# Kernel optimization log

Measured on AMD Instinct MI355X. Metric: run time of the kernel, lower is better.

The kernel has to match this reference:

```python
import jax, jax.numpy as jnp
import numpy as np

NUM_EMBEDDINGS = 1024
EMBEDDING_DIM = 512
COMMITMENT_COST = 0.25


def setup_inputs() -> dict:
    key = jax.random.key(0)
    k1, k2 = jax.random.split(key)
    inputs = jax.random.normal(k1, (128, 512, EMBEDDING_DIM), dtype=jnp.float32)
    # torch init: uniform_(-1/K, 1/K)
    emb_weight = jax.random.uniform(
        k2, (NUM_EMBEDDINGS, EMBEDDING_DIM), dtype=jnp.float32,
        minval=-1.0 / NUM_EMBEDDINGS, maxval=1.0 / NUM_EMBEDDINGS)
    return {"inputs": inputs, "emb_weight": emb_weight}


def reference(inputs, emb_weight):
    K, D = emb_weight.shape
    flat = inputs.reshape(-1, D)  # [N, D]
    # squared euclidean distances to every code: [N, K]
    distances = (jnp.sum(flat * flat, axis=1, keepdims=True)
                 + jnp.sum(emb_weight * emb_weight, axis=1)
                 - 2.0 * jnp.matmul(flat, emb_weight.T))
    encoding_indices = jnp.argmin(distances, axis=1)  # [N]
    encodings = jax.nn.one_hot(encoding_indices, K, dtype=inputs.dtype)  # [N, K]
    # matmul(one_hot, W) == gather; use gather (same math, efficient form)
    quantized = jnp.take(emb_weight, encoding_indices, axis=0).reshape(inputs.shape)
    e_latent_loss = jnp.mean((jax.lax.stop_gradient(quantized) - inputs) ** 2)
    q_latent_loss = jnp.mean((quantized - jax.lax.stop_gradient(inputs)) ** 2)
    loss = q_latent_loss + COMMITMENT_COST * e_latent_loss
    # straight-through estimator
    quantized_st = inputs + jax.lax.stop_gradient(quantized - inputs)
    avg_probs = jnp.mean(encodings, axis=0)
    perplexity = jnp.exp(-jnp.sum(avg_probs * jnp.log(avg_probs + 1e-10)))
    return (loss, quantized_st, perplexity, encodings)
```

## Files before the change

kernel.cpp:

```cpp
#include <hip/hip_runtime.h>
#include <stdint.h>

typedef unsigned short u16;
typedef unsigned long long u64;
using short8 = __attribute__((ext_vector_type(8))) short;
using f32x16 = __attribute__((ext_vector_type(16))) float;
using f32x4v = __attribute__((ext_vector_type(4))) float;

#define NROWS 65536
#define DIM   512
#define KC    1024

#define GLOBAL_AS __attribute__((address_space(1)))
#define LDS_AS    __attribute__((address_space(3)))

__device__ __forceinline__ void gload_lds16(const void* g, void* l) {
  __builtin_amdgcn_global_load_lds((const GLOBAL_AS uint32_t*)g,
                                   (LDS_AS uint32_t*)l, 16, 0, 0);
}

__device__ __forceinline__ u16 f2bf(float f) {
  unsigned u = __float_as_uint(f);
  return (u16)((u + 0x7fffu + ((u >> 16) & 1u)) >> 16);
}

__device__ __forceinline__ f32x4v ntload4(const float* p) {
  return __builtin_nontemporal_load((const f32x4v*)p);
}
__device__ __forceinline__ void ntstore4(float* p, f32x4v v) {
  __builtin_nontemporal_store(v, (f32x4v*)p);
}

__global__ __launch_bounds__(256) void wprep_kernel(const float* __restrict__ W,
                                                    short8* __restrict__ WhT8,
                                                    float* __restrict__ wnorm,
                                                    int* __restrict__ counts,
                                                    double* __restrict__ sums) {
  if (blockIdx.x == 0) {
    for (int k = threadIdx.x; k < KC; k += 256) counts[k] = 0;
    if (threadIdx.x < 2) sums[threadIdx.x] = 0.0;
  }
  int code = blockIdx.x * 4 + (threadIdx.x >> 6);
  int l = threadIdx.x & 63;
  const float* wr = W + (size_t)code * DIM + l * 8;
  float4 v0 = *(const float4*)wr;
  float4 v1 = *(const float4*)(wr + 4);
  float s = v0.x * v0.x + v0.y * v0.y + v0.z * v0.z + v0.w * v0.w
          + v1.x * v1.x + v1.y * v1.y + v1.z * v1.z + v1.w * v1.w;
  short8 pk;
  pk[0] = (short)f2bf(v0.x); pk[1] = (short)f2bf(v0.y);
  pk[2] = (short)f2bf(v0.z); pk[3] = (short)f2bf(v0.w);
  pk[4] = (short)f2bf(v1.x); pk[5] = (short)f2bf(v1.y);
  pk[6] = (short)f2bf(v1.z); pk[7] = (short)f2bf(v1.w);
  WhT8[(size_t)(code >> 5) * 2048 + (l >> 1) * 64 + (l & 1) * 32 + (code & 31)] = pk;
#pragma unroll
  for (int off = 32; off; off >>= 1) s += __shfl_xor(s, off, 64);
  if (l == 0) wnorm[code] = s;
}

__global__ __launch_bounds__(256)
__attribute__((amdgpu_waves_per_eu(2, 2))) void mm_kernel(
    const float* __restrict__ X, const u16* __restrict__ WhTf,
    const float* __restrict__ wnorm, int* __restrict__ best_idx,
    int* __restrict__ counts, double* __restrict__ sums,
    float* __restrict__ encf) {
  __shared__ __align__(16) u16 BsU[2][16384];
  __shared__ double sdbl[4];
  const int t = threadIdx.x;
  const int w = t >> 6, l = t & 63;
  const int r = l & 31, h = l >> 5;
  const int row0 = blockIdx.x * 128;

#pragma unroll
  for (int i = 0; i < 8; ++i)
    gload_lds16(WhTf + i * 2048 + t * 8, &BsU[0][i * 2048 + t * 8]);

  const float* Xr = X + (size_t)(row0 + w * 32 + r) * DIM + h * 8;
  short8 aF[32];
  double xacc = 0.0;
#pragma unroll
  for (int s = 0; s < 32; ++s) {
    f32x4v v0 = ntload4(Xr + s * 16);
    f32x4v v1 = ntload4(Xr + s * 16 + 4);
    xacc += (double)v0[0] * v0[0] + (double)v0[1] * v0[1] + (double)v0[2] * v0[2] + (double)v0[3] * v0[3]
          + (double)v1[0] * v1[0] + (double)v1[1] * v1[1] + (double)v1[2] * v1[2] + (double)v1[3] * v1[3];
    short8 pk;
    pk[0] = (short)f2bf(v0[0]); pk[1] = (short)f2bf(v0[1]);
    pk[2] = (short)f2bf(v0[2]); pk[3] = (short)f2bf(v0[3]);
    pk[4] = (short)f2bf(v1[0]); pk[5] = (short)f2bf(v1[1]);
    pk[6] = (short)f2bf(v1[2]); pk[7] = (short)f2bf(v1[3]);
    aF[s] = pk;
  }
#pragma unroll
  for (int off = 32; off; off >>= 1) xacc += __shfl_xor(xacc, off, 64);
  if (l == 0) atomicAdd(&sums[0], xacc);

  unsigned best_[16];
#pragma unroll
  for (int q = 0; q < 16; ++q) best_[q] = 0xFFFFFFFFu;

  f32x4v* encz = (f32x4v*)(encf + (size_t)row0 * KC);
  const f32x4v zero4 = {0.f, 0.f, 0.f, 0.f};

  asm volatile("s_waitcnt vmcnt(0)" ::: "memory");
  __builtin_amdgcn_s_barrier();
  __builtin_amdgcn_sched_barrier(0);

  for (int kt = 0; kt < 32; ++kt) {
    const int buf = kt & 1;
    if (kt < 31) {
      const u16* src = WhTf + (size_t)(kt + 1) * 16384;
#pragma unroll
      for (int i = 0; i < 8; ++i)
        gload_lds16(src + i * 2048 + t * 8, &BsU[buf ^ 1][i * 2048 + t * 8]);
    }
#pragma unroll
    for (int j = 0; j < 4; ++j)
      __builtin_nontemporal_store(zero4, &encz[kt * 1024 + j * 256 + t]);

    const u16* bufp = &BsU[buf][l * 8];
    short8 bv[8];
#pragma unroll
    for (int i = 0; i < 8; ++i) bv[i] = *(const short8*)&bufp[i * 512];
    f32x16 acc_e = {}, acc_o = {};
#pragma unroll
    for (int ks = 0; ks < 32; ++ks) {
      if (ks & 1)
        acc_o = __builtin_amdgcn_mfma_f32_32x32x16_bf16(aF[ks], bv[ks & 7], acc_o, 0, 0, 0);
      else
        acc_e = __builtin_amdgcn_mfma_f32_32x32x16_bf16(aF[ks], bv[ks & 7], acc_e, 0, 0, 0);
      if (ks < 24) bv[ks & 7] = *(const short8*)&bufp[(ks + 8) * 512];
    }
    float wn = wnorm[kt * 32 + r];
    unsigned col = (unsigned)(kt * 32 + r);
#pragma unroll
    for (int q = 0; q < 16; ++q) {
      float sc = fmaf(-2.0f, acc_e[q] + acc_o[q], wn);
      unsigned u_ = __float_as_uint(sc);
      unsigned key = (u_ & 0x80000000u) ? ~u_ : (u_ | 0x80000000u);
      best_[q] = min(best_[q], (key & 0xFFFFFC00u) | col);
    }
    asm volatile("s_waitcnt vmcnt(4)" ::: "memory");
    __builtin_amdgcn_s_barrier();
    __builtin_amdgcn_sched_barrier(0);
  }

  double local = 0.0;
#pragma unroll
  for (int q = 0; q < 16; ++q) {
    unsigned pb = best_[q];
#pragma unroll
    for (int off = 16; off; off >>= 1)
      pb = min(pb, (unsigned)__shfl_xor((int)pb, off, 32));
    if (r == 0) {
      int row = row0 + w * 32 + (q & 3) + 8 * (q >> 2) + 4 * h;
      int k = (int)(pb & 1023u);
      best_idx[row] = k;
      atomicAdd(&counts[k], 1);
      unsigned key = (pb & 0xFFFFFC00u) | 0x200u;
      unsigned uu = (key & 0x80000000u) ? (key ^ 0x80000000u) : ~key;
      local += (double)__uint_as_float(uu);
    }
  }
  {
    double o32 = __shfl(local, 32, 64);
    if (l == 0) sdbl[w] = local + o32;
  }
  __syncthreads();
  if (t == 0) atomicAdd(&sums[1], sdbl[0] + sdbl[1] + sdbl[2] + sdbl[3]);
}

__global__ __launch_bounds__(256) void out_kernel(const float* __restrict__ W,
                                                  const int* __restrict__ best_idx,
                                                  float* __restrict__ out,
                                                  float* __restrict__ encf) {
  const int t = threadIdx.x;
  const int w = t >> 6, l = t & 63;
#pragma unroll
  for (int j = 0; j < 8; ++j) {
    int rr = blockIdx.x * 32 + w * 8 + j;
    int k = best_idx[rr];
    const float* Wr = W + (size_t)k * DIM;
    size_t ob = (size_t)rr * DIM;
    {
      f32x4v cm = *(const f32x4v*)(Wr + 4 * l);
      f32x4v c1 = *(const f32x4v*)(Wr + 4 * l + 4);
      f32x4v sv = {cm[3], c1[0], c1[1], c1[2]};
      ntstore4(out + ob + 4 + 4 * l, sv);
    }
    if (l <= 62) {
      int m = l + 64;
      f32x4v dm = *(const f32x4v*)(Wr + 4 * m);
      f32x4v d1 = *(const f32x4v*)(Wr + 4 * m + 4);
      f32x4v sv = {dm[3], d1[0], d1[1], d1[2]};
      ntstore4(out + ob + 4 + 4 * m, sv);
    }
    if (l < 3) out[ob + 1 + l] = Wr[l];
    if (l == 3) out[ob + 512] = Wr[511];
    if (l == 4) encf[(size_t)rr * KC + k] = 1.0f;
  }
}

__global__ __launch_bounds__(256) void finalize_kernel(
    const int* __restrict__ counts, const double* __restrict__ sums,
    float* __restrict__ out_loss, float* __restrict__ out_perp) {
  __shared__ float red[4];
  int t = threadIdx.x;
  float h = 0.f;
  for (int k = t; k < KC; k += 256) {
    float p = (float)counts[k] / (float)NROWS;
    h -= p * logf(p + 1e-10f);
  }
#pragma unroll
  for (int off = 32; off; off >>= 1) h += __shfl_xor(h, off, 64);
  if ((t & 63) == 0) red[t >> 6] = h;
  __syncthreads();
  if (t == 0) {
    float H = red[0] + red[1] + red[2] + red[3];
    *out_perp = expf(H);
    double m = (sums[0] + sums[1]) / (double)((long long)NROWS * DIM);
    *out_loss = (float)(1.25 * m);
  }
}

extern "C" void kernel_launch(void* const* d_in, const int* in_sizes, int n_in,
                              void* d_out, int out_size, void* d_ws, size_t ws_size,
                              hipStream_t stream) {
  const float* X = (const float*)d_in[0];
  const float* W = (const float*)d_in[1];
  float* out = (float*)d_out;
  char* ws = (char*)d_ws;

  float* out_loss = out;
  float* out_perp = out + 1 + NROWS * DIM;
  float* encf     = out + 2 + NROWS * DIM;

  short8* WhT8    = (short8*)ws;
  float*  wnorm   = (float*)(ws + (1040u << 10));
  int*    counts  = (int*)(ws + (1040u << 10) + 4096);
  double* sums    = (double*)(ws + (1040u << 10) + 8192);
  int*    best_idx= (int*)(ws + (1040u << 10) + 12288);

  wprep_kernel<<<KC / 4, 256, 0, stream>>>(W, WhT8, wnorm, counts, sums);
  mm_kernel<<<NROWS / 128, 256, 0, stream>>>(X, (const u16*)WhT8, wnorm,
                                             best_idx, counts, sums, encf);
  out_kernel<<<NROWS / 32, 256, 0, stream>>>(W, best_idx, out, encf);
  finalize_kernel<<<1, 256, 0, stream>>>(counts, sums, out_loss, out_perp);
}
```

Baseline: 189.5 us.

## Split codebook across blocks with 128x128 tiles and atomicMin argmin merge

Restructures the distance GEMM so each block computes a 128-row by 128-code tile with 16x16x32 MFMAs, staging both X (as swizzled bf16) and W in LDS per 64-wide K step, instead of keeping a whole row strip in registers and sweeping all codes. Partial argmins are merged across blocks with atomicMin on packed keys, and a new post kernel does the counts and loss sum. The point is more parallelism and occupancy (8x more blocks, 3 waves per EU), at the cost of re-reading X eight times, converting it to bf16 redundantly, an extra memset and launch, and global atomics.

```diff
diff --git a/kernel.cpp b/kernel.cpp
--- a/kernel.cpp
+++ b/kernel.cpp
@@ -2,9 +2,7 @@
 #include <stdint.h>
 
 typedef unsigned short u16;
-typedef unsigned long long u64;
 using short8 = __attribute__((ext_vector_type(8))) short;
-using f32x16 = __attribute__((ext_vector_type(16))) float;
 using f32x4v = __attribute__((ext_vector_type(4))) float;
 
 #define NROWS 65536
@@ -24,9 +22,6 @@
   return (u16)((u + 0x7fffu + ((u >> 16) & 1u)) >> 16);
 }
 
-__device__ __forceinline__ f32x4v ntload4(const float* p) {
-  return __builtin_nontemporal_load((const f32x4v*)p);
-}
 __device__ __forceinline__ void ntstore4(float* p, f32x4v v) {
   __builtin_nontemporal_store(v, (f32x4v*)p);
 }
@@ -52,126 +47,154 @@
   pk[2] = (short)f2bf(v0.z); pk[3] = (short)f2bf(v0.w);
   pk[4] = (short)f2bf(v1.x); pk[5] = (short)f2bf(v1.y);
   pk[6] = (short)f2bf(v1.z); pk[7] = (short)f2bf(v1.w);
-  WhT8[(size_t)(code >> 5) * 2048 + (l >> 1) * 64 + (l & 1) * 32 + (code & 31)] = pk;
+  WhT8[(size_t)(code >> 4) * 1024 + (size_t)(l >> 2) * 64 +
+       (size_t)(l & 3) * 16 + (code & 15)] = pk;
 #pragma unroll
   for (int off = 32; off; off >>= 1) s += __shfl_xor(s, off, 64);
   if (l == 0) wnorm[code] = s;
 }
 
-__global__ __launch_bounds__(256)
-__attribute__((amdgpu_waves_per_eu(2, 2))) void mm_kernel(
+__global__ __launch_bounds__(256, 3) void mm_kernel(
     const float* __restrict__ X, const u16* __restrict__ WhTf,
-    const float* __restrict__ wnorm, int* __restrict__ best_idx,
-    int* __restrict__ counts, double* __restrict__ sums,
-    float* __restrict__ encf) {
-  __shared__ __align__(16) u16 BsU[2][16384];
-  __shared__ double sdbl[4];
+    const float* __restrict__ wnorm, unsigned* __restrict__ wsBest,
+    double* __restrict__ sums, float* __restrict__ encf) {
+  __shared__ __align__(16) u16 As[128 * 64];
+  __shared__ __align__(16) u16 Bs[8 * 1024];
+  __shared__ unsigned mbuf[2][64];
+  __shared__ float sflt[4];
   const int t = threadIdx.x;
   const int w = t >> 6, l = t & 63;
-  const int r = l & 31, h = l >> 5;
-  const int row0 = blockIdx.x * 128;
-
-#pragma unroll
-  for (int i = 0; i < 8; ++i)
-    gload_lds16(WhTf + i * 2048 + t * 8, &BsU[0][i * 2048 + t * 8]);
-
-  const float* Xr = X + (size_t)(row0 + w * 32 + r) * DIM + h * 8;
-  short8 aF[32];
-  double xacc = 0.0;
-#pragma unroll
-  for (int s = 0; s < 32; ++s) {
-    f32x4v v0 = ntload4(Xr + s * 16);
-    f32x4v v1 = ntload4(Xr + s * 16 + 4);
-    xacc += (double)v0[0] * v0[0] + (double)v0[1] * v0[1] + (double)v0[2] * v0[2] + (double)v0[3] * v0[3]
-          + (double)v1[0] * v1[0] + (double)v1[1] * v1[1] + (double)v1[2] * v1[2] + (double)v1[3] * v1[3];
-    short8 pk;
-    pk[0] = (short)f2bf(v0[0]); pk[1] = (short)f2bf(v0[1]);
-    pk[2] = (short)f2bf(v0[2]); pk[3] = (short)f2bf(v0[3]);
-    pk[4] = (short)f2bf(v1[0]); pk[5] = (short)f2bf(v1[1]);
-    pk[6] = (short)f2bf(v1[2]); pk[7] = (short)f2bf(v1[3]);
-    aF[s] = pk;
-  }
-#pragma unroll
-  for (int off = 32; off; off >>= 1) xacc += __shfl_xor(xacc, off, 64);
-  if (l == 0) atomicAdd(&sums[0], xacc);
-
-  unsigned best_[16];
-#pragma unroll
-  for (int q = 0; q < 16; ++q) best_[q] = 0xFFFFFFFFu;
-
-  f32x4v* encz = (f32x4v*)(encf + (size_t)row0 * KC);
-  const f32x4v zero4 = {0.f, 0.f, 0.f, 0.f};
-
-  asm volatile("s_waitcnt vmcnt(0)" ::: "memory");
-  __builtin_amdgcn_s_barrier();
-  __builtin_amdgcn_sched_barrier(0);
-
-  for (int kt = 0; kt < 32; ++kt) {
-    const int buf = kt & 1;
-    if (kt < 31) {
-      const u16* src = WhTf + (size_t)(kt + 1) * 16384;
-#pragma unroll
-      for (int i = 0; i < 8; ++i)
-        gload_lds16(src + i * 2048 + t * 8, &BsU[buf ^ 1][i * 2048 + t * 8]);
-    }
-#pragma unroll
-    for (int j = 0; j < 4; ++j)
-      __builtin_nontemporal_store(zero4, &encz[kt * 1024 + j * 256 + t]);
-
-    const u16* bufp = &BsU[buf][l * 8];
-    short8 bv[8];
-#pragma unroll
-    for (int i = 0; i < 8; ++i) bv[i] = *(const short8*)&bufp[i * 512];
-    f32x16 acc_e = {}, acc_o = {};
-#pragma unroll
-    for (int ks = 0; ks < 32; ++ks) {
-      if (ks & 1)
-        acc_o = __builtin_amdgcn_mfma_f32_32x32x16_bf16(aF[ks], bv[ks & 7], acc_o, 0, 0, 0);
-      else
-        acc_e = __builtin_amdgcn_mfma_f32_32x32x16_bf16(aF[ks], bv[ks & 7], acc_e, 0, 0, 0);
-      if (ks < 24) bv[ks & 7] = *(const short8*)&bufp[(ks + 8) * 512];
-    }
-    float wn = wnorm[kt * 32 + r];
-    unsigned col = (unsigned)(kt * 32 + r);
-#pragma unroll
-    for (int q = 0; q < 16; ++q) {
-      float sc = fmaf(-2.0f, acc_e[q] + acc_o[q], wn);
-      unsigned u_ = __float_as_uint(sc);
-      unsigned key = (u_ & 0x80000000u) ? ~u_ : (u_ | 0x80000000u);
-      best_[q] = min(best_[q], (key & 0xFFFFFC00u) | col);
-    }
-    asm volatile("s_waitcnt vmcnt(4)" ::: "memory");
-    __builtin_amdgcn_s_barrier();
-    __builtin_amdgcn_sched_barrier(0);
-  }
-
-  double local = 0.0;
-#pragma unroll
-  for (int q = 0; q < 16; ++q) {
-    unsigned pb = best_[q];
-#pragma unroll
-    for (int off = 16; off; off >>= 1)
-      pb = min(pb, (unsigned)__shfl_xor((int)pb, off, 32));
-    if (r == 0) {
-      int row = row0 + w * 32 + (q & 3) + 8 * (q >> 2) + 4 * h;
-      int k = (int)(pb & 1023u);
-      best_idx[row] = k;
-      atomicAdd(&counts[k], 1);
-      unsigned key = (pb & 0xFFFFFC00u) | 0x200u;
-      unsigned uu = (key & 0x80000000u) ? (key ^ 0x80000000u) : ~key;
-      local += (double)__uint_as_float(uu);
-    }
-  }
-  {
-    double o32 = __shfl(local, 32, 64);
-    if (l == 0) sdbl[w] = local + o32;
-  }
+  const int wr = w >> 1, wc = w & 1;
+  const int xcd = blockIdx.x & 7;
+  const int j = blockIdx.x >> 3;
+  const int cb = j & 7;
+  const int strip = xcd + 8 * (j >> 3);
+  const int row0 = strip * 128;
+
+  const int row_l = t >> 1;
+  const int koff = (t & 1) * 32;
+
+  f32x4v acc[4][4] = {};
+  float xpart = 0.f;
+
+  for (int step = 0; step < 8; ++step) {
+    const float* as_ = X + (size_t)(row0 + row_l) * DIM + step * 64 + koff;
+    f32x4v av[8];
+#pragma unroll
+    for (int jj = 0; jj < 4; ++jj) {
+      av[2 * jj] = *(const f32x4v*)(as_ + jj * 8);
+      av[2 * jj + 1] = *(const f32x4v*)(as_ + jj * 8 + 4);
+    }
+#pragma unroll
+    for (int i = 0; i < 4; ++i) {
+      int chunk = i * 2 + (t >> 7);
+      gload_lds16(WhTf + (size_t)(cb * 8 + chunk) * 8192 + step * 1024 + (t & 127) * 8,
+                  &Bs[chunk * 1024 + (t & 127) * 8]);
+    }
+    {
+      int erow = row0 + step * 16 + (t >> 4);
+      float* ep = encf + (size_t)erow * KC + cb * 128 + (t & 15) * 8;
+      const f32x4v z4 = {0.f, 0.f, 0.f, 0.f};
+      ntstore4(ep, z4);
+      ntstore4(ep + 4, z4);
+    }
+    if (cb == 0) {
+#pragma unroll
+      for (int v = 0; v < 8; ++v)
+        xpart += av[v][0] * av[v][0] + av[v][1] * av[v][1] +
+                 av[v][2] * av[v][2] + av[v][3] * av[v][3];
+    }
+#pragma unroll
+    for (int jj = 0; jj < 4; ++jj) {
+      short8 pk;
+      pk[0] = (short)f2bf(av[2 * jj][0]); pk[1] = (short)f2bf(av[2 * jj][1]);
+      pk[2] = (short)f2bf(av[2 * jj][2]); pk[3] = (short)f2bf(av[2 * jj][3]);
+      pk[4] = (short)f2bf(av[2 * jj + 1][0]); pk[5] = (short)f2bf(av[2 * jj + 1][1]);
+      pk[6] = (short)f2bf(av[2 * jj + 1][2]); pk[7] = (short)f2bf(av[2 * jj + 1][3]);
+      int slot = (t & 1) * 4 + jj;
+      *(short8*)&As[row_l * 64 + ((slot ^ (row_l & 7)) * 8)] = pk;
+    }
+    __syncthreads();
+
+#pragma unroll
+    for (int ks = 0; ks < 2; ++ks) {
+      short8 af[4], bf[4];
+#pragma unroll
+      for (int m = 0; m < 4; ++m) {
+        int row = wr * 64 + m * 16 + (l & 15);
+        af[m] = *(const short8*)&As[row * 64 + (((ks * 4 + (l >> 4)) ^ (row & 7)) * 8)];
+      }
+#pragma unroll
+      for (int n = 0; n < 4; ++n)
+        bf[n] = *(const short8*)&Bs[(wc * 4 + n) * 1024 + ks * 512 + l * 8];
+#pragma unroll
+      for (int m = 0; m < 4; ++m)
+#pragma unroll
+        for (int n = 0; n < 4; ++n)
+          acc[m][n] = __builtin_amdgcn_mfma_f32_16x16x32_bf16(af[m], bf[n], acc[m][n], 0, 0, 0);
+    }
+    __syncthreads();
+  }
+
+  if (cb == 0) {
+    float xs = xpart;
+#pragma unroll
+    for (int off = 32; off; off >>= 1) xs += __shfl_xor(xs, off, 64);
+    if (l == 0) sflt[w] = xs;
+  }
+  unsigned pbv[16];
+#pragma unroll
+  for (int m = 0; m < 4; ++m)
+#pragma unroll
+    for (int r = 0; r < 4; ++r) {
+      unsigned pb = 0xFFFFFFFFu;
+#pragma unroll
+      for (int n = 0; n < 4; ++n) {
+        int col = cb * 128 + wc * 64 + n * 16 + (l & 15);
+        float sc = fmaf(-2.0f, acc[m][n][r], wnorm[col]);
+        unsigned u_ = __float_as_uint(sc);
+        unsigned key = (u_ & 0x80000000u) ? ~u_ : (u_ | 0x80000000u);
+        pb = min(pb, (key & 0xFFFFFC00u) | (unsigned)col);
+      }
+#pragma unroll
+      for (int off = 8; off; off >>= 1)
+        pb = min(pb, (unsigned)__shfl_xor((int)pb, off, 16));
+      pbv[m * 4 + r] = pb;
+      if (wc == 1 && (l & 15) == 0)
+        mbuf[wr][m * 16 + (l >> 4) * 4 + r] = pb;
+    }
   __syncthreads();
-  if (t == 0) atomicAdd(&sums[1], sdbl[0] + sdbl[1] + sdbl[2] + sdbl[3]);
+  if (cb == 0 && t == 0)
+    atomicAdd(&sums[0], (double)(sflt[0] + sflt[1] + sflt[2] + sflt[3]));
+  if (wc == 0 && (l & 15) == 0) {
+#pragma unroll
+    for (int m = 0; m < 4; ++m)
+#pragma unroll
+      for (int r = 0; r < 4; ++r) {
+        int rl = m * 16 + (l >> 4) * 4 + r;
+        unsigned pb = min(pbv[m * 4 + r], mbuf[wr][rl]);
+        atomicMin(&wsBest[row0 + wr * 64 + rl], pb);
+      }
+  }
+}
+
+__global__ __launch_bounds__(256) void post_kernel(const unsigned* __restrict__ wsBest,
+                                                   int* __restrict__ counts,
+                                                   double* __restrict__ sums) {
+  int i = blockIdx.x * 256 + threadIdx.x;
+  unsigned pb = wsBest[i];
+  int k = (int)(pb & 1023u);
+  atomicAdd(&counts[k], 1);
+  unsigned key = (pb & 0xFFFFFC00u) | 0x200u;
+  unsigned uu = (key & 0x80000000u) ? (key ^ 0x80000000u) : ~key;
+  double d = (double)__uint_as_float(uu);
+#pragma unroll
+  for (int off = 32; off; off >>= 1) d += __shfl_xor(d, off, 64);
+  if ((threadIdx.x & 63) == 0) atomicAdd(&sums[1], d);
 }
 
 __global__ __launch_bounds__(256) void out_kernel(const float* __restrict__ W,
-                                                  const int* __restrict__ best_idx,
+                                                  const unsigned* __restrict__ wsBest,
                                                   float* __restrict__ out,
                                                   float* __restrict__ encf) {
   const int t = threadIdx.x;
@@ -179,7 +202,7 @@
 #pragma unroll
   for (int j = 0; j < 8; ++j) {
     int rr = blockIdx.x * 32 + w * 8 + j;
-    int k = best_idx[rr];
+    int k = (int)(wsBest[rr] & 1023u);
     const float* Wr = W + (size_t)k * DIM;
     size_t ob = (size_t)rr * DIM;
     {
@@ -235,15 +258,17 @@
   float* out_perp = out + 1 + NROWS * DIM;
   float* encf     = out + 2 + NROWS * DIM;
 
-  short8* WhT8    = (short8*)ws;
-  float*  wnorm   = (float*)(ws + (1040u << 10));
-  int*    counts  = (int*)(ws + (1040u << 10) + 4096);
-  double* sums    = (double*)(ws + (1040u << 10) + 8192);
-  int*    best_idx= (int*)(ws + (1040u << 10) + 12288);
-
+  short8*   WhT8   = (short8*)ws;
+  float*    wnorm  = (float*)(ws + (1024u << 10));
+  int*      counts = (int*)(ws + (1024u << 10) + 4096);
+  double*   sums   = (double*)(ws + (1024u << 10) + 8192);
+  unsigned* wsBest = (unsigned*)(ws + (1024u << 10) + 12288);
+
+  hipMemsetAsync(wsBest, 0xFF, NROWS * sizeof(unsigned), stream);
   wprep_kernel<<<KC / 4, 256, 0, stream>>>(W, WhT8, wnorm, counts, sums);
-  mm_kernel<<<NROWS / 128, 256, 0, stream>>>(X, (const u16*)WhT8, wnorm,
-                                             best_idx, counts, sums, encf);
-  out_kernel<<<NROWS / 32, 256, 0, stream>>>(W, best_idx, out, encf);
+  mm_kernel<<<(NROWS / 128) * 8, 256, 0, stream>>>(X, (const u16*)WhT8, wnorm,
+                                                   wsBest, sums, encf);
+  post_kernel<<<NROWS / 256, 256, 0, stream>>>(wsBest, counts, sums);
+  out_kernel<<<NROWS / 32, 256, 0, stream>>>(W, wsBest, out, encf);
   finalize_kernel<<<1, 256, 0, stream>>>(counts, sums, out_loss, out_perp);
 }
```

Result: slower. 244.8 us (+29.2%).
